# Kernel tuning notes

Measured on AMD Instinct MI355X. Metric: run time of the kernel, lower is better.

Reference implementation:

```python
import jax, jax.numpy as jnp
import numpy as np
import math

MAX_ATOMS = 50
B = 2048
D = 512            # node_hidden_dim
MA = 512           # mol_a_repr_dim
ATT = 128          # attention dim
HID = 256          # mlp hidden width


def _counts():
    return (np.arange(B) % MAX_ATOMS) + 1  # deterministic ragged counts, sum = 52176


def _lin_params(key, din, dout):
    k1, k2 = jax.random.split(key)
    lim = 1.0 / math.sqrt(din)
    w = jax.random.uniform(k1, (din, dout), jnp.float32, -lim, lim)
    b = jax.random.uniform(k2, (dout,), jnp.float32, -lim, lim)
    return w, b


def mlp2(x, w1, b1, w2, b2):
    # create_mlp(in, out, [hidden]) => Linear -> ReLU -> Linear
    return jax.nn.relu(x @ w1 + b1) @ w2 + b2


def setup_inputs() -> dict:
    key = jax.random.key(0)
    ks = jax.random.split(key, 16)
    counts = _counts()
    N = int(counts.sum())  # 52176
    inp = {
        'mol_a_reprs': jax.random.normal(ks[0], (B, MA), jnp.float32),
        'node_hiddens': jax.random.normal(ks[1], (N, D), jnp.float32),
        'batch_counts': jnp.asarray(counts, jnp.int32),
    }
    wq1, bq1 = _lin_params(ks[2], D, HID); wq2, bq2 = _lin_params(ks[3], HID, ATT)
    wk1, bk1 = _lin_params(ks[4], D, HID); wk2, bk2 = _lin_params(ks[5], HID, ATT)
    wv1, bv1 = _lin_params(ks[6], D, HID); wv2, bv2 = _lin_params(ks[7], HID, ATT)
    uk1, ubk1 = _lin_params(ks[8], ATT, HID); uk2, ubk2 = _lin_params(ks[9], HID, ATT)
    uq1, ubq1 = _lin_params(ks[10], MA, HID); uq2, ubq2 = _lin_params(ks[11], HID, ATT)
    cs1, bcs1 = _lin_params(ks[12], MAX_ATOMS, 128); cs2, bcs2 = _lin_params(ks[13], 128, MAX_ATOMS)
    inp.update(dict(wq1=wq1, bq1=bq1, wq2=wq2, bq2=bq2,
                    wk1=wk1, bk1=bk1, wk2=wk2, bk2=bk2,
                    wv1=wv1, bv1=bv1, wv2=wv2, bv2=bv2,
                    uk1=uk1, ubk1=ubk1, uk2=uk2, ubk2=ubk2,
                    uq1=uq1, ubq1=ubq1, uq2=uq2, ubq2=ubq2,
                    cs1=cs1, bcs1=bcs1, cs2=cs2, bcs2=bcs2))
    return inp


def reference(mol_a_reprs, node_hiddens, batch_counts,
              wq1, bq1, wq2, bq2, wk1, bk1, wk2, bk2, wv1, bv1, wv2, bv2,
              uk1, ubk1, uk2, ubk2, uq1, ubq1, uq2, ubq2,
              cs1, bcs1, cs2, bcs2):
    N = node_hiddens.shape[0]
    offsets = jnp.concatenate([jnp.zeros((1,), jnp.int32),
                               jnp.cumsum(batch_counts)[:-1].astype(jnp.int32)])
    pos = jnp.arange(MAX_ATOMS, dtype=jnp.int32)                     # (M,)
    valid = pos[None, :] < batch_counts[:, None]                      # (B, M)
    gidx = jnp.clip(offsets[:, None] + pos[None, :], 0, N - 1)        # (B, M)
    # ragged gather -> padded (B, M, D), zeros at pad slots
    inp = jnp.where(valid[:, :, None], node_hiddens[gidx], 0.0)
    mask = ~valid                                                     # True where padded

    K = mlp2(inp, wk1, bk1, wk2, bk2)                                 # (B, M, 128)
    Q = mlp2(inp, wq1, bq1, wq2, bq2)
    V = mlp2(inp, wv1, bv1, wv2, bv2)
    KQT = jnp.einsum('bmd,bnd->bmn', K, Q)                            # (B, M, M)
    KQT = jnp.where(mask[:, :, None] | mask[:, None, :], -1e9, KQT)
    attn = jax.nn.softmax(KQT / math.sqrt(ATT), axis=-1)
    corr = jnp.einsum('bmn,bnd->bmd', attn, V)                        # (B, M, 128)

    K2 = mlp2(corr, uk1, ubk1, uk2, ubk2)                             # (B, M, 128)
    Q2 = mlp2(mol_a_reprs, uq1, ubq1, uq2, ubq2)                      # (B, 128)
    logits = jnp.einsum('bmd,bd->bm', K2, Q2) / math.sqrt(ATT)        # (B, M)
    sel = jax.nn.sigmoid(mlp2(logits, cs1, bcs1, cs2, bcs2))          # (B, M)

    # ragged scatter back to (N,); pad slots routed to dummy slot N
    sidx = jnp.where(valid, offsets[:, None] + pos[None, :], N)
    out = jnp.zeros((N + 1,), sel.dtype).at[sidx.reshape(-1)].set(sel.reshape(-1))
    return out[:N]
```

## Files before the change

kernel.cpp:

```cpp
#include <hip/hip_runtime.h>
#include <hip/hip_bf16.h>
#include <math.h>

#define DIM   512
#define HIDW  256
#define ATTW  128
#define MAXC  50
#define BLK   256
#define KW    128
#define HLW   128
#define HL2   264
#define BUFW  136
#define SB_W  52
#define CH    10
#define PXR   32
#define SCL   0.08838834764831845f

#define SWZ(row, e) ((e) ^ (((row) & 7) << 3))

#define AT_PA 12800
#define AT_KB 19200
#define AT_SM 32000

typedef float f32x4 __attribute__((ext_vector_type(4)));
typedef short s16x8 __attribute__((ext_vector_type(8)));

__device__ __forceinline__ float bf2f(ushort u){ union{unsigned i;float f;}v; v.i=((unsigned)u)<<16; return v.f; }
__device__ __forceinline__ ushort f2bf(float f){
  union{float f;unsigned i;}v; v.f=f;
  unsigned r = v.i + 0x7fffu + ((v.i>>16)&1u);
  return (ushort)(r>>16);
}
__device__ __forceinline__ s16x8 ldfrag(const ushort* p){ s16x8 v; __builtin_memcpy(&v, p, 16); return v; }
__device__ __forceinline__ f32x4 mfma16(s16x8 a, s16x8 b, f32x4 c){
  return __builtin_amdgcn_mfma_f32_16x16x32_bf16(a, b, c, 0, 0, 0);
}
__device__ __forceinline__ const ushort* fragp(const ushort* Wf, int ntile, int ktile, int KT, int L){
  return Wf + (((size_t)ntile*KT + ktile)*64 + L)*8;
}

template<bool F32>
__device__ __forceinline__ float ld(const void* p, int i){
  if (F32) return ((const float*)p)[i];
  return bf2f(((const ushort*)p)[i]);
}

struct P27 {
  const void *molA, *nodeH; const int* counts;
  const void *wq1,*bq1,*wq2,*bq2, *wk1,*bk1,*wk2,*bk2, *wv1,*bv1,*wv2,*bv2;
  const void *uk1,*ubk1,*uk2,*ubk2, *uq1,*ubq1,*uq2,*ubq2;
  const void *cs1,*bcs1,*cs2,*bcs2;
  void* out;
};

#define O_WK1T 0
#define O_WQ1T 131072
#define O_WV1T 262144
#define O_WK2T 393216
#define O_WQ2T 425984
#define O_WV2T 458752
#define O_UK1T 491520
#define O_UK2T 524288
#define WT_ELEMS   557056
#define O_UQ1TT 557056
#define O_UQ2TT 688128
#define WT2_ELEMS  720896
#define WT_T2ELEMS 393216
#define WT_BYTE_OFF 8704
#define Q2_BYTE_OFF (WT_BYTE_OFF + WT2_ELEMS*2)

__device__ __forceinline__ int detect_f32m(const ushort* molAu, int t, int* cntSh)
{
  if (t == 0) *cntSh = 0;
  __syncthreads();
  int e = (molAu[t] >> 7) & 0xFF;
  if (e >= 100 && e <= 140) atomicAdd(cntSh, 1);
  __syncthreads();
  return (*cntSh >= 220) ? 0 : 1;
}

__global__ void prep_kernel(const ushort* __restrict__ molAu,
                            const int* __restrict__ counts, int nb,
                            int* __restrict__ wsInt)
{
  __shared__ int part[BLK];
  __shared__ int cnt;
  const int t = threadIdx.x;
  if (t == 0) cnt = 0;
  __syncthreads();
  int e = (molAu[t] >> 7) & 0xFF;
  if (e >= 100 && e <= 140) atomicAdd(&cnt, 1);
  const int per = (nb + BLK - 1) / BLK;
  int s = 0;
  for (int i = 0; i < per; i++) { int idx = t*per + i; if (idx < nb) s += counts[idx]; }
  part[t] = s;
  __syncthreads();
  if (t == 0) {
    int run = 0;
    for (int i = 0; i < BLK; i++) { int v = part[i]; part[i] = run; run += v; }
    wsInt[0] = (cnt >= 220) ? 0 : 1;
  }
  __syncthreads();
  int run = part[t];
  for (int i = 0; i < per; i++) {
    int idx = t*per + i;
    if (idx < nb) { wsInt[4 + idx] = run; run += counts[idx]; }
  }
}

__global__ void prep2_kernel(P27 P, const int* __restrict__ counts, int nb,
                             int* __restrict__ wsInt,
                             ushort* __restrict__ wt, unsigned long long cap_elems,
                             unsigned nwt)
{
  __shared__ int shInt[BLK];
  const int t = threadIdx.x;
  const unsigned bid = blockIdx.x;

  if (bid == nwt) {
    __shared__ int cnt;
    if (t == 0) cnt = 0;
    __syncthreads();
    int e = (((const ushort*)P.molA)[t] >> 7) & 0xFF;
    if (e >= 100 && e <= 140) atomicAdd(&cnt, 1);
    const int per = (nb + BLK - 1) / BLK;
    int s = 0;
    for (int i = 0; i < per; i++) { int idx = t*per + i; if (idx < nb) s += counts[idx]; }
    shInt[t] = s;
    __syncthreads();
    if (t == 0) {
      int run = 0;
      for (int i = 0; i < BLK; i++) { int v = shInt[i]; shInt[i] = run; run += v; }
      wsInt[0] = (cnt >= 220) ? 0 : 1;
    }
    __syncthreads();
    int run = shInt[t];
    for (int i = 0; i < per; i++) {
      int idx = t*per + i;
      if (idx < nb) { wsInt[4 + idx] = run; run += counts[idx]; }
    }
    return;
  }

  const int f32m = detect_f32m((const ushort*)P.molA, t, &shInt[0]);
  unsigned i = bid*BLK + t;
  if (i >= WT2_ELEMS) return;
  if ((unsigned long long)i >= cap_elems) return;
  const void* src; unsigned j; int K, ldw;
  if (i < O_WK2T) {
    int m = i / 131072; j = i - m*131072;
    src = (m==0) ? P.wk1 : ((m==1) ? P.wq1 : P.wv1);
    K = 512; ldw = HIDW;
  } else if (i < O_UK1T) {
    int m = (i - O_WK2T) / 32768; j = (i - O_WK2T) - m*32768;
    src = (m==0) ? P.wk2 : ((m==1) ? P.wq2 : P.wv2);
    K = 256; ldw = ATTW;
  } else if (i < O_UK2T) {
    j = i - O_UK1T; src = P.uk1;  K = 128; ldw = HIDW;
  } else if (i < O_UQ1TT) {
    j = i - O_UK2T; src = P.uk2;  K = 256; ldw = ATTW;
  } else if (i < O_UQ2TT) {
    j = i - O_UQ1TT; src = P.uq1; K = 512; ldw = HIDW;
  } else {
    j = i - O_UQ2TT; src = P.uq2; K = 256; ldw = ATTW;
  }
  int tile = j >> 9, within = j & 511;
  int Lp = within >> 3, jj = within & 7;
  int l16 = Lp & 15, quad = Lp >> 4;
  int KT = K >> 5;
  int ntile = tile / KT, ktile = tile - ntile*KT;
  int n = ntile*16 + l16;
  int k = ktile*32 + quad*8 + jj;
  int idx = k*ldw + n;
  float v = f32m ? ((const float*)src)[idx] : bf2f(((const ushort*)src)[idx]);
  wt[i] = f2bf(v);
}

__global__ void __launch_bounds__(BLK, 3)
proj_kernel(P27 P, const int* __restrict__ wsInt, const ushort* __restrict__ wt,
            ushort* __restrict__ kqv, float* __restrict__ q2ws,
            long Nrows, int nb, int ntX)
{
  __shared__ __align__(16) ushort xs [PXR*DIM];
  __shared__ __align__(16) ushort hid[PXR*HIDW];
  const int t = threadIdx.x, bid = blockIdx.x;
  const int f32m = wsInt[0];
  const long NP = Nrows * ATTW;
  const bool isml = (bid >= ntX);
  const long r0 = isml ? (long)(bid - ntX)*PXR : (long)bid*PXR;
  int rows;
  const void* X;
  if (isml) { int rem = nb - (int)r0;        rows = (rem < PXR) ? rem : PXR; X = P.molA; }
  else      { long rem = Nrows - r0;         rows = (rem < PXR) ? (int)rem : PXR; X = P.nodeH; }
  if (rows <= 0) return;

  for (int i = t*8; i < PXR*DIM; i += BLK*8) {
    int row = i >> 9;
    int e   = i & (DIM-1);
    s16x8 o = {};
    if (row < rows) {
      if (f32m) {
        const float* xp = (const float*)X + (r0 + row)*DIM + e;
        f32x4 v0, v1; __builtin_memcpy(&v0, xp, 16); __builtin_memcpy(&v1, xp+4, 16);
#pragma unroll
        for (int q = 0; q < 4; q++) { o[q] = (short)f2bf(v0[q]); o[4+q] = (short)f2bf(v1[q]); }
      } else {
        o = ldfrag((const ushort*)X + (r0 + row)*DIM + e);
      }
    }
    __builtin_memcpy(&xs[row*DIM + SWZ(row, e)], &o, 16);
  }
  __syncthreads();

  const int w = t >> 6, L = t & 63, quad = L >> 4, l16 = L & 15;
  const int nsets = isml ? 1 : 3;
  for (int si = 0; si < nsets; si++) {
    const ushort *W1t, *W2t; const void *b1, *b2;
    if (isml)        { W1t = wt+O_UQ1TT; b1 = P.ubq1; W2t = wt+O_UQ2TT; b2 = P.ubq2; }
    else if (si==0)  { W1t = wt+O_WK1T;  b1 = P.bk1;  W2t = wt+O_WK2T;  b2 = P.bk2;  }
    else if (si==1)  { W1t = wt+O_WQ1T;  b1 = P.bq1;  W2t = wt+O_WQ2T;  b2 = P.bq2;  }
    else             { W1t = wt+O_WV1T;  b1 = P.bv1;  W2t = wt+O_WV2T;  b2 = P.bv2;  }

    f32x4 acc[2][4];
#pragma unroll
    for (int i = 0; i < 2; i++)
#pragma unroll
      for (int jn = 0; jn < 4; jn++) acc[i][jn] = (f32x4){0.f,0.f,0.f,0.f};
#pragma unroll 2
    for (int k0 = 0; k0 < DIM; k0 += 32) {
      const int kt = k0 >> 5;
      const int eo = SWZ(l16, k0 + quad*8);
      s16x8 a0 = ldfrag(xs + l16*DIM + eo);
      s16x8 a1 = ldfrag(xs + (16 + l16)*DIM + eo);
#pragma unroll
      for (int nt = 0; nt < 4; nt++) {
        s16x8 b = ldfrag(fragp(W1t, w*4 + nt, kt, 16, L));
        acc[0][nt] = mfma16(a0, b, acc[0][nt]);
        acc[1][nt] = mfma16(a1, b, acc[1][nt]);
      }
    }
    __syncthreads();
#pragma unroll
    for (int nt = 0; nt < 4; nt++) {
      int col = w*64 + nt*16 + l16;
      float bb = f32m ? ((const float*)b1)[col] : bf2f(((const ushort*)b1)[col]);
#pragma unroll
      for (int mt = 0; mt < 2; mt++)
#pragma unroll
        for (int r = 0; r < 4; r++) {
          int row = mt*16 + quad*4 + r;
          hid[row*HIDW + SWZ(row, col)] = f2bf(fmaxf(acc[mt][nt][r] + bb, 0.f));
        }
    }
    __syncthreads();

    f32x4 acc2[2][2];
#pragma unroll
    for (int i = 0; i < 2; i++) { acc2[i][0] = (f32x4){0.f,0.f,0.f,0.f}; acc2[i][1] = (f32x4){0.f,0.f,0.f,0.f}; }
#pragma unroll 2
    for (int k0 = 0; k0 < HIDW; k0 += 32) {
      const int kt = k0 >> 5;
      const int eo = SWZ(l16, k0 + quad*8);
      s16x8 a0 = ldfrag(hid + l16*HIDW + eo);
      s16x8 a1 = ldfrag(hid + (16 + l16)*HIDW + eo);
      s16x8 b0 = ldfrag(fragp(W2t, w*2,     kt, 8, L));
      s16x8 b1v= ldfrag(fragp(W2t, w*2 + 1, kt, 8, L));
      acc2[0][0] = mfma16(a0, b0,  acc2[0][0]);
      acc2[0][1] = mfma16(a0, b1v, acc2[0][1]);
      acc2[1][0] = mfma16(a1, b0,  acc2[1][0]);
      acc2[1][1] = mfma16(a1, b1v, acc2[1][1]);
    }
#pragma unroll
    for (int nt = 0; nt < 2; nt++) {
      int col = w*32 + nt*16 + l16;
      float bb = f32m ? ((const float*)b2)[col] : bf2f(((const ushort*)b2)[col]);
#pragma unroll
      for (int mt = 0; mt < 2; mt++)
#pragma unroll
        for (int r = 0; r < 4; r++) {
          int row = mt*16 + quad*4 + r;
          if (row < rows) {
            float v = acc2[mt][nt][r] + bb;
            if (isml) q2ws[(r0 + row)*ATTW + col] = v;
            else      kqv[(size_t)si*NP + (r0 + row)*ATTW + col] = f2bf(v);
          }
        }
    }
  }
}


__device__ __forceinline__ void scores_g(const ushort* __restrict__ Kp,
                                         const ushort* __restrict__ Qp,
                                         long offset, int c,
                                         float* __restrict__ sb, int t)
{
  const int w = t >> 6, L = t & 63, quad = L >> 4, l16 = L & 15;
  f32x4 acc[4];
#pragma unroll
  for (int i = 0; i < 4; i++) acc[i] = (f32x4){0.f,0.f,0.f,0.f};
  const int col = w*16 + l16;
  const long gq = offset + ((col < c) ? col : 0);
  long ga[4];
#pragma unroll
  for (int mt = 0; mt < 4; mt++) {
    int row = mt*16 + l16;
    ga[mt] = offset + ((row < c) ? row : 0);
  }
  __builtin_amdgcn_s_setprio(1);
#pragma unroll
  for (int k0 = 0; k0 < ATTW; k0 += 32) {
    s16x8 b = ldfrag(Qp + (size_t)gq*ATTW + k0 + quad*8);
#pragma unroll
    for (int mt = 0; mt < 4; mt++) {
      s16x8 a = ldfrag(Kp + (size_t)ga[mt]*ATTW + k0 + quad*8);
      acc[mt] = mfma16(a, b, acc[mt]);
    }
  }
  __builtin_amdgcn_s_setprio(0);
#pragma unroll
  for (int mt = 0; mt < 4; mt++)
#pragma unroll
    for (int r = 0; r < 4; r++) {
      int row = mt*16 + quad*4 + r;
      if (row < MAXC && col < MAXC)
        sb[row*SB_W + col] = (row < c && col < c) ? acc[mt][r]*SCL : -1e9f*SCL;
    }
}

__device__ __forceinline__ void softmax_pa(float* __restrict__ sb,
                                           ushort* __restrict__ pa, int c, int t)
{
  const int m = t >> 2, j = t & 3;
  if (m < MAXC) {
    float* row = sb + m*SB_W;
    float mx = -3.4e38f;
    for (int n = j; n < MAXC; n += 4) mx = fmaxf(mx, row[n]);
    mx = fmaxf(mx, __shfl_xor(mx, 1));
    mx = fmaxf(mx, __shfl_xor(mx, 2));
    float sum = 0.f;
    for (int n = j; n < MAXC; n += 4) { float e = expf(row[n] - mx); row[n] = e; sum += e; }
    sum += __shfl_xor(sum, 1);
    sum += __shfl_xor(sum, 2);
    float inv = 1.f / sum;
    for (int n = j; n < 64; n += 4)
      pa[m*64 + SWZ(m, n)] = (n < MAXC) ? f2bf(row[n] * inv) : (ushort)0;
  }
}

__device__ __forceinline__ void corr_half(const ushort* __restrict__ pa,
                                          const ushort* __restrict__ vt,
                                          ushort* __restrict__ dst, int colbase, int t)
{
  const int w = t >> 6, L = t & 63, quad = L >> 4, l16 = L & 15;
  f32x4 acc[4];
#pragma unroll
  for (int i = 0; i < 4; i++) acc[i] = (f32x4){0.f,0.f,0.f,0.f};
  const int dr = w*16 + l16;
  __builtin_amdgcn_s_setprio(1);
#pragma unroll
  for (int k0 = 0; k0 < 64; k0 += 32) {
    s16x8 b = ldfrag(vt + dr*64 + SWZ(dr, k0 + quad*8));
#pragma unroll
    for (int mt = 0; mt < 4; mt++) {
      int row = mt*16 + l16;
      int ar = (row < MAXC) ? row : 0;
      s16x8 a = ldfrag(pa + ar*64 + SWZ(ar, k0 + quad*8));
      acc[mt] = mfma16(a, b, acc[mt]);
    }
  }
  __builtin_amdgcn_s_setprio(0);
  const int col = colbase + w*16 + l16;
#pragma unroll
  for (int mt = 0; mt < 4; mt++)
#pragma unroll
    for (int r = 0; r < 4; r++) {
      int row = mt*16 + quad*4 + r;
      if (row < MAXC)
        dst[row*KW + SWZ(row, col)] = f2bf(acc[mt][r]);
    }
}

template<bool F32>
__device__ __forceinline__ void s1l_half(const ushort* __restrict__ src,
                                         const ushort* __restrict__ W1t,
                                         const void* __restrict__ Bv,
                                         ushort* __restrict__ hl, int t, int h)
{
  const int w = t >> 6, L = t & 63, quad = L >> 4, l16 = L & 15;
  f32x4 acc[4][2];
#pragma unroll
  for (int i = 0; i < 4; i++) { acc[i][0] = (f32x4){0.f,0.f,0.f,0.f}; acc[i][1] = (f32x4){0.f,0.f,0.f,0.f}; }
  __builtin_amdgcn_s_setprio(1);
#pragma unroll
  for (int k0 = 0; k0 < ATTW; k0 += 32) {
    const int kt = k0 >> 5;
    s16x8 b0 = ldfrag(fragp(W1t, h*8 + w*2,     kt, 4, L));
    s16x8 b1 = ldfrag(fragp(W1t, h*8 + w*2 + 1, kt, 4, L));
#pragma unroll
    for (int mt = 0; mt < 4; mt++) {
      int row = mt*16 + l16;
      int ar = (row < MAXC) ? row : 0;
      s16x8 a = ldfrag(src + ar*KW + SWZ(ar, k0 + quad*8));
      acc[mt][0] = mfma16(a, b0, acc[mt][0]);
      acc[mt][1] = mfma16(a, b1, acc[mt][1]);
    }
  }
  __builtin_amdgcn_s_setprio(0);
#pragma unroll
  for (int nt = 0; nt < 2; nt++) {
    int lcol = w*32 + nt*16 + l16;
    float bb = ld<F32>(Bv, h*128 + lcol);
#pragma unroll
    for (int mt = 0; mt < 4; mt++)
#pragma unroll
      for (int r = 0; r < 4; r++) {
        int row = mt*16 + quad*4 + r;
        if (row < MAXC)
          hl[row*HLW + SWZ(row, lcol)] = f2bf(fmaxf(acc[mt][nt][r] + bb, 0.f));
      }
  }
}

template<bool F32>
__device__ __forceinline__ void s2_partial(const ushort* __restrict__ hl,
                                           const ushort* __restrict__ W2t,
                                           int h, f32x4 (&acc)[4][2], int t)
{
  const int w = t >> 6, L = t & 63, quad = L >> 4, l16 = L & 15;
  __builtin_amdgcn_s_setprio(1);
#pragma unroll
  for (int k0 = 0; k0 < 128; k0 += 32) {
    const int kt = h*4 + (k0 >> 5);
    s16x8 b0 = ldfrag(fragp(W2t, w*2,     kt, 8, L));
    s16x8 b1 = ldfrag(fragp(W2t, w*2 + 1, kt, 8, L));
#pragma unroll
    for (int mt = 0; mt < 4; mt++) {
      int row = mt*16 + l16;
      int ar = (row < MAXC) ? row : 0;
      s16x8 a = ldfrag(hl + ar*HLW + SWZ(ar, k0 + quad*8));
      acc[mt][0] = mfma16(a, b0, acc[mt][0]);
      acc[mt][1] = mfma16(a, b1, acc[mt][1]);
    }
  }
  __builtin_amdgcn_s_setprio(0);
}

template<bool F32>
__device__ __forceinline__ void s2_store(f32x4 (&acc)[4][2], const void* __restrict__ Bv,
                                         ushort* __restrict__ dst, int t)
{
  const int w = t >> 6, L = t & 63, quad = L >> 4, l16 = L & 15;
#pragma unroll
  for (int nt = 0; nt < 2; nt++) {
    int col = w*32 + nt*16 + l16;
    float bb = ld<F32>(Bv, col);
#pragma unroll
    for (int mt = 0; mt < 4; mt++)
#pragma unroll
      for (int r = 0; r < 4; r++) {
        int row = mt*16 + quad*4 + r;
        if (row < MAXC)
          dst[row*KW + SWZ(row, col)] = f2bf(acc[mt][nt][r] + bb);
      }
  }
}

template<bool F32>
__device__ void attn_body(const P27& P, int b, int t, char* smem,
                          long offset, int c,
                          const ushort* __restrict__ wt,
                          const ushort* __restrict__ Kp, const ushort* __restrict__ Qp,
                          const ushort* __restrict__ Vp, const float* __restrict__ q2ws)
{
  float*  sb = (float*)smem;
  ushort* vt = (ushort*)smem;
  ushort* hl = (ushort*)smem;
  ushort* pa = (ushort*)(smem + AT_PA);
  ushort* kb = (ushort*)(smem + AT_KB);
  float* q2   = (float*)smem;
  float* lgt  = (float*)(smem + 512);
  float* selh = (float*)(smem + 768);

  scores_g(Kp, Qp, offset, c, sb, t);
  __syncthreads();
  softmax_pa(sb, pa, c, t);
  __syncthreads();

#pragma unroll
  for (int half = 0; half < 2; half++) {
    for (int i = t; i < 512; i += BLK) {
      int atom = i & 63, chunk = i >> 6;
      s16x8 f = {};
      if (atom < c) f = ldfrag(Vp + (size_t)(offset + atom)*ATTW + half*64 + chunk*8);
#pragma unroll
      for (int j = 0; j < 8; j++) {
        int d = chunk*8 + j;
        vt[d*64 + SWZ(d, atom)] = (ushort)f[j];
      }
    }
    __syncthreads();
    corr_half(pa, vt, kb, half*64, t);
    __syncthreads();
  }

  {
    f32x4 acc[4][2];
#pragma unroll
    for (int i = 0; i < 4; i++) { acc[i][0] = (f32x4){0.f,0.f,0.f,0.f}; acc[i][1] = (f32x4){0.f,0.f,0.f,0.f}; }
    s1l_half<F32>(kb, wt + O_UK1T, P.ubk1, hl, t, 0); __syncthreads();
    s2_partial<F32>(hl, wt + O_UK2T, 0, acc, t);      __syncthreads();
    s1l_half<F32>(kb, wt + O_UK1T, P.ubk1, hl, t, 1); __syncthreads();
    s2_partial<F32>(hl, wt + O_UK2T, 1, acc, t);
    s2_store<F32>(acc, P.ubk2, kb, t);
    __syncthreads();
  }

  if (t < ATTW) q2[t] = q2ws[(size_t)b*ATTW + t];
  __syncthreads();
  if (t < MAXC) {
    float s = 0.f;
    for (int k = 0; k < ATTW; k++)
      s += bf2f(kb[t*KW + SWZ(t, k)]) * q2[k];
    lgt[t] = s * SCL;
  }
  __syncthreads();
  if (t < ATTW) {
    float a = 0.f;
    for (int k = 0; k < MAXC; k++)
      a += lgt[k] * ld<F32>(P.cs1, k*ATTW + t);
    selh[t] = fmaxf(a + ld<F32>(P.bcs1, t), 0.f);
  }
  __syncthreads();
  if (t < c) {
    float a = 0.f;
    for (int k = 0; k < ATTW; k++)
      a += selh[k] * ld<F32>(P.cs2, k*MAXC + t);
    a += ld<F32>(P.bcs2, t);
    float v = 1.f / (1.f + expf(-a));
    if (F32) ((float*)P.out)[offset + t] = v;
    else     ((ushort*)P.out)[offset + t] = f2bf(v);
  }
}

__global__ void __launch_bounds__(BLK, 5)
attn_kernel(P27 P, const int* __restrict__ wsInt, const ushort* __restrict__ wt,
            const ushort* __restrict__ kqv, const float* __restrict__ q2ws, long Nrows)
{
  __shared__ __align__(16) char smem[AT_SM];
  const int t = threadIdx.x, b = blockIdx.x;
  const int f32m = wsInt[0];
  const long offset = wsInt[4 + b];
  const int c = P.counts[b];
  const long NP = Nrows * ATTW;
  const ushort* Kp = kqv;
  const ushort* Qp = kqv + NP;
  const ushort* Vp = kqv + 2*NP;
  if (f32m) attn_body<true >(P, b, t, smem, offset, c, wt, Kp, Qp, Vp, q2ws);
  else      attn_body<false>(P, b, t, smem, offset, c, wt, Kp, Qp, Vp, q2ws);
}

template<bool F32, bool XB>
__device__ __forceinline__ void stage1_mfma(const void* __restrict__ X, int xb, int c,
                                            const ushort* __restrict__ Wt,
                                            const void* __restrict__ Bv,
                                            ushort* __restrict__ hl, int hls, int t,
                                            int wlim)
{
  const int w = t >> 6, L = t & 63, quad = L >> 4, l16 = L & 15;
  f32x4 acc[4][4];
#pragma unroll
  for (int i = 0; i < 4; i++)
#pragma unroll
    for (int j = 0; j < 4; j++) acc[i][j] = (f32x4){0.f,0.f,0.f,0.f};

  bool va[4]; int rr[4];
#pragma unroll
  for (int mt = 0; mt < 4; mt++) {
    int row = mt*16 + l16;
    va[mt] = (row < c);
    rr[mt] = va[mt] ? row : 0;
  }

#pragma unroll 2
  for (int k0 = 0; k0 < DIM; k0 += 32) {
    const int kt = k0 >> 5;
    s16x8 a[4];
#pragma unroll
    for (int mt = 0; mt < 4; mt++) {
      s16x8 z = {};
      if (va[mt]) {
        if (XB || !F32) {
          a[mt] = ldfrag((const ushort*)X + xb + rr[mt]*DIM + k0 + quad*8);
        } else {
          const float* xp = (const float*)X + xb + rr[mt]*DIM + k0 + quad*8;
          f32x4 v0, v1;
          __builtin_memcpy(&v0, xp, 16);
          __builtin_memcpy(&v1, xp+4, 16);
          s16x8 v;
#pragma unroll
          for (int j = 0; j < 4; j++) { v[j] = (short)f2bf(v0[j]); v[4+j] = (short)f2bf(v1[j]); }
          a[mt] = v;
        }
      } else a[mt] = z;
    }
#pragma unroll
    for (int nt = 0; nt < 4; nt++) {
      s16x8 b = ldfrag(fragp(Wt, w*4 + nt, kt, 16, L));
#pragma unroll
      for (int mt = 0; mt < 4; mt++)
        acc[mt][nt] = mfma16(a[mt], b, acc[mt][nt]);
    }
  }
#pragma unroll
  for (int nt = 0; nt < 4; nt++) {
    int col = w*64 + nt*16 + l16;
    float bb = ld<F32>(Bv, col);
#pragma unroll
    for (int mt = 0; mt < 4; mt++)
#pragma unroll
      for (int r = 0; r < 4; r++) {
        int row = mt*16 + quad*4 + r;
        if (row < wlim)
          hl[row*hls + col] = f2bf(fmaxf(acc[mt][nt][r] + bb, 0.f));
      }
  }
}

template<bool F32>
__device__ void stage1_g(const void* X, int xb, int c,
                         const void* W, const void* Bv, ushort* hl, int t)
{
  for (int r0 = 0; r0 < MAXC; r0 += CH) {
    float acc[CH];
#pragma unroll
    for (int i = 0; i < CH; i++) acc[i] = 0.f;
    for (int k = 0; k < DIM; k++) {
      float wv = ld<F32>(W, k*HIDW + t);
#pragma unroll
      for (int i = 0; i < CH; i++) {
        int m = r0 + i;
        int mc = (m < c) ? m : 0;
        float xv = ld<F32>(X, xb + mc*DIM + k);
        acc[i] += ((m < c) ? xv : 0.f) * wv;
      }
    }
    float bb = ld<F32>(Bv, t);
#pragma unroll
    for (int i = 0; i < CH; i++)
      hl[(r0+i)*HIDW + t] = f2bf(fmaxf(acc[i] + bb, 0.f));
  }
}

template<bool F32>
__device__ void stage1_l(const ushort* S, const void* W, const void* Bv,
                         ushort* hl, int t)
{
  for (int r0 = 0; r0 < MAXC; r0 += CH) {
    float acc[CH];
#pragma unroll
    for (int i = 0; i < CH; i++) acc[i] = 0.f;
    for (int k = 0; k < ATTW; k++) {
      float wv = ld<F32>(W, k*HIDW + t);
#pragma unroll
      for (int i = 0; i < CH; i++)
        acc[i] += bf2f(S[(r0+i)*BUFW + k]) * wv;
    }
    float bb = ld<F32>(Bv, t);
#pragma unroll
    for (int i = 0; i < CH; i++)
      hl[(r0+i)*HIDW + t] = f2bf(fmaxf(acc[i] + bb, 0.f));
  }
}

template<bool F32>
__device__ void stage2(const void* W, const void* Bv, const ushort* hlp,
                       ushort* dst, int t)
{
  const int col = t & (ATTW-1);
  const int h = t >> 7;
  float bb = ld<F32>(Bv, col);
  for (int m = h; m < MAXC; m += 2) {
    float a = 0.f;
    for (int k = 0; k < HIDW; k++)
      a += bf2f(hlp[m*HIDW + k]) * ld<F32>(W, k*ATTW + col);
    dst[m*BUFW + col] = f2bf(a + bb);
  }
}

template<bool F32, bool MF>
__device__ void body(const P27& P, int b, int t,
                     ushort* hl, ushort* buf0, ushort* buf1, float* sb,
                     float* q2h, float* q2, float* logit, float* selh,
                     int offset, int c, const ushort* wt)
{
  const int xb = offset * DIM;

  if (MF) stage1_mfma<F32,false>(P.nodeH, xb, c, wt + O_WK1T, P.bk1, hl, HIDW, t, MAXC);
  else    stage1_g<F32>(P.nodeH, xb, c, P.wk1, P.bk1, hl, t);
  __syncthreads();
  stage2<F32>(P.wk2, P.bk2, hl, buf0, t);
  __syncthreads();
  if (MF) stage1_mfma<F32,false>(P.nodeH, xb, c, wt + O_WQ1T, P.bq1, hl, HIDW, t, MAXC);
  else    stage1_g<F32>(P.nodeH, xb, c, P.wq1, P.bq1, hl, t);
  __syncthreads();
  stage2<F32>(P.wq2, P.bq2, hl, buf1, t);
  __syncthreads();

  for (int idx = t; idx < MAXC*MAXC; idx += BLK) {
    int m = idx / MAXC, n = idx - m*MAXC;
    float s;
    if (m < c && n < c) {
      s = 0.f;
      for (int k = 0; k < ATTW; k++)
        s += bf2f(buf0[m*BUFW + k]) * bf2f(buf1[n*BUFW + k]);
    } else s = -1e9f;
    sb[m*SB_W + n] = s * SCL;
  }
  __syncthreads();
  if (t < MAXC) {
    float* row = sb + t*SB_W;
    float mx = row[0];
    for (int n = 1; n < MAXC; n++) mx = fmaxf(mx, row[n]);
    float sum = 0.f;
    for (int n = 0; n < MAXC; n++) { float e = expf(row[n] - mx); row[n] = e; sum += e; }
    float inv = 1.f / sum;
    for (int n = 0; n < MAXC; n++) row[n] *= inv;
  }
  __syncthreads();

  if (MF) stage1_mfma<F32,false>(P.nodeH, xb, c, wt + O_WV1T, P.bv1, hl, HIDW, t, MAXC);
  else    stage1_g<F32>(P.nodeH, xb, c, P.wv1, P.bv1, hl, t);
  __syncthreads();
  stage2<F32>(P.wv2, P.bv2, hl, buf0, t);
  __syncthreads();

  {
    const int col = t & (ATTW-1);
    const int h = t >> 7;
    for (int m = h; m < MAXC; m += 2) {
      float a = 0.f;
      for (int n = 0; n < MAXC; n++)
        a += sb[m*SB_W + n] * bf2f(buf0[n*BUFW + col]);
      buf1[m*BUFW + col] = f2bf(a);
    }
  }
  __syncthreads();

  stage1_l<F32>(buf1, P.uk1, P.ubk1, hl, t);
  __syncthreads();
  stage2<F32>(P.uk2, P.ubk2, hl, buf0, t);
  __syncthreads();

  {
    float a = 0.f;
    for (int k = 0; k < DIM; k++)
      a += ld<F32>(P.molA, b*DIM + k) * ld<F32>(P.uq1, k*HIDW + t);
    q2h[t] = fmaxf(a + ld<F32>(P.ubq1, t), 0.f);
  }
  __syncthreads();
  if (t < ATTW) {
    float a = 0.f;
    for (int k = 0; k < HIDW; k++)
      a += q2h[k] * ld<F32>(P.uq2, k*ATTW + t);
    q2[t] = a + ld<F32>(P.ubq2, t);
  }
  __syncthreads();
  if (t < MAXC) {
    float s = 0.f;
    for (int k = 0; k < ATTW; k++)
      s += bf2f(buf0[t*BUFW + k]) * q2[k];
    logit[t] = s * SCL;
  }
  __syncthreads();
  if (t < ATTW) {
    float a = 0.f;
    for (int k = 0; k < MAXC; k++)
      a += logit[k] * ld<F32>(P.cs1, k*ATTW + t);
    selh[t] = fmaxf(a + ld<F32>(P.bcs1, t), 0.f);
  }
  __syncthreads();
  if (t < c) {
    float a = 0.f;
    for (int k = 0; k < ATTW; k++)
      a += selh[k] * ld<F32>(P.cs2, k*MAXC + t);
    a += ld<F32>(P.bcs2, t);
    float v = 1.f / (1.f + expf(-a));
    if (F32) ((float*)P.out)[offset + t] = v;
    else     ((ushort*)P.out)[offset + t] = f2bf(v);
  }
}

__global__ void fused_mfma(P27 P, const int* __restrict__ wsInt, const ushort* __restrict__ wt)
{
  __shared__ __align__(16) ushort hl  [MAXC*HIDW];
  __shared__ __align__(16) ushort buf0[MAXC*BUFW];
  __shared__ __align__(16) ushort buf1[MAXC*BUFW];
  __shared__ __align__(16) float  sb  [MAXC*SB_W];
  __shared__ __align__(16) float  q2h [HIDW];
  __shared__ __align__(16) float  q2  [ATTW];
  __shared__ __align__(16) float  logit[64];
  __shared__ __align__(16) float  selh[ATTW];
  const int t = threadIdx.x, b = blockIdx.x;
  const int f32m = wsInt[0];
  const int offset = wsInt[4 + b];
  const int c = P.counts[b];
  if (f32m) body<true , true>(P, b, t, hl, buf0, buf1, sb, q2h, q2, logit, selh, offset, c, wt);
  else      body<false, true>(P, b, t, hl, buf0, buf1, sb, q2h, q2, logit, selh, offset, c, wt);
}

__global__ void fused_scalar(P27 P, const int* __restrict__ wsInt)
{
  __shared__ __align__(16) ushort hl  [MAXC*HIDW];
  __shared__ __align__(16) ushort buf0[MAXC*BUFW];
  __shared__ __align__(16) ushort buf1[MAXC*BUFW];
  __shared__ __align__(16) float  sb  [MAXC*SB_W];
  __shared__ __align__(16) float  q2h [HIDW];
  __shared__ __align__(16) float  q2  [ATTW];
  __shared__ __align__(16) float  logit[64];
  __shared__ __align__(16) float  selh[ATTW];
  const int t = threadIdx.x, b = blockIdx.x;
  const int f32m = wsInt[0];
  const int offset = wsInt[4 + b];
  const int c = P.counts[b];
  if (f32m) body<true , false>(P, b, t, hl, buf0, buf1, sb, q2h, q2, logit, selh, offset, c, nullptr);
  else      body<false, false>(P, b, t, hl, buf0, buf1, sb, q2h, q2, logit, selh, offset, c, nullptr);
}

extern "C" void kernel_launch(void* const* d_in, const int* in_sizes, int n_in,
                              void* d_out, int out_size, void* d_ws, size_t ws_size,
                              hipStream_t stream) {
  P27 P;
  P.molA  = d_in[0];
  P.nodeH = d_in[1];
  P.counts= (const int*)d_in[2];
  P.wq1 = d_in[3];  P.bq1 = d_in[4];  P.wq2 = d_in[5];  P.bq2 = d_in[6];
  P.wk1 = d_in[7];  P.bk1 = d_in[8];  P.wk2 = d_in[9];  P.bk2 = d_in[10];
  P.wv1 = d_in[11]; P.bv1 = d_in[12]; P.wv2 = d_in[13]; P.bv2 = d_in[14];
  P.uk1 = d_in[15]; P.ubk1= d_in[16]; P.uk2 = d_in[17]; P.ubk2= d_in[18];
  P.uq1 = d_in[19]; P.ubq1= d_in[20]; P.uq2 = d_in[21]; P.ubq2= d_in[22];
  P.cs1 = d_in[23]; P.bcs1= d_in[24]; P.cs2 = d_in[25]; P.bcs2= d_in[26];
  P.out = d_out;
  const int nb = in_sizes[2];
  int* wsInt = (int*)d_ws;

  const long xelems = (long)in_sizes[1];
  const long Nrows  = xelems / DIM;
  const int  ntX = (int)((Nrows + PXR - 1) / PXR);
  const int  ntA = (nb + PXR - 1) / PXR;

  size_t q2_off  = (size_t)Q2_BYTE_OFF;
  size_t kqv_off = (q2_off + (size_t)nb * ATTW * 4 + 255) & ~(size_t)255;
  const size_t need_new = kqv_off + (size_t)3 * Nrows * ATTW * 2;
  const size_t need2    = (size_t)WT_BYTE_OFF + (size_t)WT_T2ELEMS * 2;

  if (ws_size >= need_new) {
    ushort* wt   = (ushort*)((char*)d_ws + WT_BYTE_OFF);
    float*  q2ws = (float*)((char*)d_ws + q2_off);
    ushort* kqv  = (ushort*)((char*)d_ws + kqv_off);
    unsigned long long cap = (ws_size - WT_BYTE_OFF) / 2;
    const unsigned nwt = (WT2_ELEMS + BLK - 1)/BLK;
    prep2_kernel<<<dim3(nwt + 1), dim3(BLK), 0, stream>>>(P, (const int*)d_in[2], nb,
                                                          wsInt, wt, cap, nwt);
    proj_kernel<<<dim3(ntX + ntA), dim3(BLK), 0, stream>>>(P, wsInt, wt, kqv, q2ws,
                                                           Nrows, nb, ntX);
    attn_kernel<<<dim3(nb), dim3(BLK), 0, stream>>>(P, wsInt, wt, kqv, q2ws, Nrows);
  } else if (ws_size >= need2) {
    ushort* wt = (ushort*)((char*)d_ws + WT_BYTE_OFF);
    unsigned long long cap = (ws_size - WT_BYTE_OFF) / 2;
    const unsigned nwt = (WT2_ELEMS + BLK - 1)/BLK;
    prep2_kernel<<<dim3(nwt + 1), dim3(BLK), 0, stream>>>(P, (const int*)d_in[2], nb,
                                                          wsInt, wt, cap, nwt);
    fused_mfma<<<dim3(nb), dim3(BLK), 0, stream>>>(P, wsInt, wt);
  } else {
    prep_kernel<<<dim3(1), dim3(BLK), 0, stream>>>((const ushort*)d_in[0],
                                                   (const int*)d_in[2], nb, wsInt);
    fused_scalar<<<dim3(nb), dim3(BLK), 0, stream>>>(P, wsInt);
  }
}
```

Measured before the change: 402.7 us.

## Split bf16 projection into per-weight-set blocks reading activations directly

Adds a projection kernel for the bf16 input mode that gives each (row tile, K/Q/V/molA set) pair its own block, instead of one block looping over all three sets. That block loads A fragments straight from global memory rather than staging the whole 32x512 tile in LDS. It drops the first-layer LDS buffer and targets higher occupancy (6 blocks per CU) with more parallel blocks. The original kernel is now restricted to the fp32 mode. In exchange, each row tile of node features is read from global memory three times, and the unused kernel still launches and exits early in each mode.

```diff
diff --git a/kernel.cpp b/kernel.cpp
--- a/kernel.cpp
+++ b/kernel.cpp
@@ -176,6 +176,103 @@
   wt[i] = f2bf(v);
 }
 
+__global__ void __launch_bounds__(BLK, 6)
+proj_set_kernel(P27 P, const int* __restrict__ wsInt, const ushort* __restrict__ wt,
+                ushort* __restrict__ kqv, float* __restrict__ q2ws,
+                long Nrows, int nb, int ntX)
+{
+  __shared__ __align__(16) ushort hid[PXR*HIDW];
+  const int t = threadIdx.x, bid = blockIdx.x;
+  const int f32m = wsInt[0];
+  if (f32m != 0) return;
+  const long NP = Nrows * ATTW;
+  const bool isml = (bid >= 3*ntX);
+  int set, rt;
+  if (!isml) { rt = bid / 3; set = bid - rt*3; }
+  else       { set = 3; rt = bid - 3*ntX; }
+  const long r0 = (long)rt * PXR;
+  int rows;
+  const ushort* X;
+  if (isml) { int rem = nb - (int)r0;  rows = (rem < PXR) ? rem : PXR;      X = (const ushort*)P.molA; }
+  else      { long rem = Nrows - r0;   rows = (rem < PXR) ? (int)rem : PXR; X = (const ushort*)P.nodeH; }
+  if (rows <= 0) return;
+  const ushort *W1t, *W2t; const void *b1, *b2;
+  switch (set) {
+    case 0: W1t = wt+O_WK1T;  b1 = P.bk1;  W2t = wt+O_WK2T;  b2 = P.bk2;  break;
+    case 1: W1t = wt+O_WQ1T;  b1 = P.bq1;  W2t = wt+O_WQ2T;  b2 = P.bq2;  break;
+    case 2: W1t = wt+O_WV1T;  b1 = P.bv1;  W2t = wt+O_WV2T;  b2 = P.bv2;  break;
+    default:W1t = wt+O_UQ1TT; b1 = P.ubq1; W2t = wt+O_UQ2TT; b2 = P.ubq2; break;
+  }
+
+  const int w = t >> 6, L = t & 63, quad = L >> 4, l16 = L & 15;
+  const long ra = r0 + ((l16      < rows) ? l16      : 0);
+  const long rb = r0 + ((16 + l16 < rows) ? 16 + l16 : 0);
+
+  f32x4 acc[2][4];
+#pragma unroll
+  for (int i = 0; i < 2; i++)
+#pragma unroll
+    for (int jn = 0; jn < 4; jn++) acc[i][jn] = (f32x4){0.f,0.f,0.f,0.f};
+#pragma unroll 2
+  for (int k0 = 0; k0 < DIM; k0 += 32) {
+    const int kt = k0 >> 5;
+    s16x8 a0 = ldfrag(X + ra*DIM + k0 + quad*8);
+    s16x8 a1 = ldfrag(X + rb*DIM + k0 + quad*8);
+#pragma unroll
+    for (int nt = 0; nt < 4; nt++) {
+      s16x8 b = ldfrag(fragp(W1t, w*4 + nt, kt, 16, L));
+      acc[0][nt] = mfma16(a0, b, acc[0][nt]);
+      acc[1][nt] = mfma16(a1, b, acc[1][nt]);
+    }
+  }
+#pragma unroll
+  for (int nt = 0; nt < 4; nt++) {
+    int col = w*64 + nt*16 + l16;
+    float bb = bf2f(((const ushort*)b1)[col]);
+#pragma unroll
+    for (int mt = 0; mt < 2; mt++)
+#pragma unroll
+      for (int r = 0; r < 4; r++) {
+        int row = mt*16 + quad*4 + r;
+        hid[row*HIDW + SWZ(row, col)] = f2bf(fmaxf(acc[mt][nt][r] + bb, 0.f));
+      }
+  }
+  __syncthreads();
+
+  f32x4 acc2[2][2];
+#pragma unroll
+  for (int i = 0; i < 2; i++) { acc2[i][0] = (f32x4){0.f,0.f,0.f,0.f}; acc2[i][1] = (f32x4){0.f,0.f,0.f,0.f}; }
+#pragma unroll 2
+  for (int k0 = 0; k0 < HIDW; k0 += 32) {
+    const int kt = k0 >> 5;
+    const int eo = SWZ(l16, k0 + quad*8);
+    s16x8 a0 = ldfrag(hid + l16*HIDW + eo);
+    s16x8 a1 = ldfrag(hid + (16 + l16)*HIDW + eo);
+    s16x8 b0 = ldfrag(fragp(W2t, w*2,     kt, 8, L));
+    s16x8 b1v= ldfrag(fragp(W2t, w*2 + 1, kt, 8, L));
+    acc2[0][0] = mfma16(a0, b0,  acc2[0][0]);
+    acc2[0][1] = mfma16(a0, b1v, acc2[0][1]);
+    acc2[1][0] = mfma16(a1, b0,  acc2[1][0]);
+    acc2[1][1] = mfma16(a1, b1v, acc2[1][1]);
+  }
+#pragma unroll
+  for (int nt = 0; nt < 2; nt++) {
+    int col = w*32 + nt*16 + l16;
+    float bb = bf2f(((const ushort*)b2)[col]);
+#pragma unroll
+    for (int mt = 0; mt < 2; mt++)
+#pragma unroll
+      for (int r = 0; r < 4; r++) {
+        int row = mt*16 + quad*4 + r;
+        if (row < rows) {
+          float v = acc2[mt][nt][r] + bb;
+          if (isml) q2ws[(r0 + row)*ATTW + col] = v;
+          else      kqv[(size_t)set*NP + (r0 + row)*ATTW + col] = f2bf(v);
+        }
+      }
+  }
+}
+
 __global__ void __launch_bounds__(BLK, 3)
 proj_kernel(P27 P, const int* __restrict__ wsInt, const ushort* __restrict__ wt,
             ushort* __restrict__ kqv, float* __restrict__ q2ws,
@@ -185,6 +282,7 @@
   __shared__ __align__(16) ushort hid[PXR*HIDW];
   const int t = threadIdx.x, bid = blockIdx.x;
   const int f32m = wsInt[0];
+  if (f32m == 0) return;
   const long NP = Nrows * ATTW;
   const bool isml = (bid >= ntX);
   const long r0 = isml ? (long)(bid - ntX)*PXR : (long)bid*PXR;
@@ -199,14 +297,10 @@
     int e   = i & (DIM-1);
     s16x8 o = {};
     if (row < rows) {
-      if (f32m) {
-        const float* xp = (const float*)X + (r0 + row)*DIM + e;
-        f32x4 v0, v1; __builtin_memcpy(&v0, xp, 16); __builtin_memcpy(&v1, xp+4, 16);
-#pragma unroll
-        for (int q = 0; q < 4; q++) { o[q] = (short)f2bf(v0[q]); o[4+q] = (short)f2bf(v1[q]); }
-      } else {
-        o = ldfrag((const ushort*)X + (r0 + row)*DIM + e);
-      }
+      const float* xp = (const float*)X + (r0 + row)*DIM + e;
+      f32x4 v0, v1; __builtin_memcpy(&v0, xp, 16); __builtin_memcpy(&v1, xp+4, 16);
+#pragma unroll
+      for (int q = 0; q < 4; q++) { o[q] = (short)f2bf(v0[q]); o[4+q] = (short)f2bf(v1[q]); }
     }
     __builtin_memcpy(&xs[row*DIM + SWZ(row, e)], &o, 16);
   }
@@ -243,7 +337,7 @@
 #pragma unroll
     for (int nt = 0; nt < 4; nt++) {
       int col = w*64 + nt*16 + l16;
-      float bb = f32m ? ((const float*)b1)[col] : bf2f(((const ushort*)b1)[col]);
+      float bb = ((const float*)b1)[col];
 #pragma unroll
       for (int mt = 0; mt < 2; mt++)
 #pragma unroll
@@ -273,7 +367,7 @@
 #pragma unroll
     for (int nt = 0; nt < 2; nt++) {
       int col = w*32 + nt*16 + l16;
-      float bb = f32m ? ((const float*)b2)[col] : bf2f(((const ushort*)b2)[col]);
+      float bb = ((const float*)b2)[col];
 #pragma unroll
       for (int mt = 0; mt < 2; mt++)
 #pragma unroll
@@ -862,6 +956,8 @@
     const unsigned nwt = (WT2_ELEMS + BLK - 1)/BLK;
     prep2_kernel<<<dim3(nwt + 1), dim3(BLK), 0, stream>>>(P, (const int*)d_in[2], nb,
                                                           wsInt, wt, cap, nwt);
+    proj_set_kernel<<<dim3(3*ntX + ntA), dim3(BLK), 0, stream>>>(P, wsInt, wt, kqv, q2ws,
+                                                                 Nrows, nb, ntX);
     proj_kernel<<<dim3(ntX + ntA), dim3(BLK), 0, stream>>>(P, wsInt, wt, kqv, q2ws,
                                                            Nrows, nb, ntX);
     attn_kernel<<<dim3(nb), dim3(BLK), 0, stream>>>(P, wsInt, wt, kqv, q2ws, Nrows);
```

Measured after the change: 403.7 us. About the same (+0.2%).
